# Performance work log

Measured on AMD Instinct MI355X. Metric: run time of the kernel, lower is better.

The kernel has to match this reference:

```python
import jax, jax.numpy as jnp
import numpy as np

B, T, D, H = 2, 2048, 2048, 16


def setup_inputs() -> dict:
    key = jax.random.key(0)
    ks = jax.random.split(key, 5)
    s = 0.02  # typical init scale
    return {
        "x": jax.random.normal(ks[0], (B, T, D), jnp.float32),
        "wq": jax.random.normal(ks[1], (D, D), jnp.float32) * s,
        "wk": jax.random.normal(ks[2], (D, D), jnp.float32) * s,
        "wv": jax.random.normal(ks[3], (D, D), jnp.float32) * s,
        "wo": jax.random.normal(ks[4], (D, D), jnp.float32) * s,
    }


def weight_quant(w):
    # BitNet ternary-ish quant: sign(w) * mean(|w|), straight-through estimator
    scale = jnp.maximum(jnp.mean(jnp.abs(w)), 1e-5)
    q = jnp.sign(w) * scale
    return jax.lax.stop_gradient(q) + w - jax.lax.stop_gradient(w)


def reference(x, wq, wk, wv, wo):
    b, t, c = x.shape
    h = H
    hd = c // h
    # F.linear: y = x @ w.T  (weight shape [out, in])
    def proj(w):
        y = jnp.einsum('btc,dc->btd', x, weight_quant(w))
        return y.reshape(b, t, h, hd).transpose(0, 2, 1, 3)  # [b,h,t,hd]

    q, k, v = proj(wq), proj(wk), proj(wv)
    scale = 1.0 / np.sqrt(hd).astype(np.float32)
    scores = jnp.einsum('bhqd,bhkd->bhqk', q, k) * scale
    causal = jnp.tril(jnp.ones((t, t), dtype=bool))
    scores = jnp.where(causal, scores, jnp.finfo(scores.dtype).min)
    att = jax.nn.softmax(scores, axis=-1)
    y = jnp.einsum('bhqk,bhkd->bhqd', att, v)
    y = y.transpose(0, 2, 1, 3).reshape(b, t, c)
    return jnp.einsum('btc,dc->btd', y, weight_quant(wo))
```

## Files before the change

### kernel.cpp

```cpp
#include <hip/hip_runtime.h>
#include <stdint.h>

#define D_MODEL 2048
#define SEQ     2048
#define BATCH   2
#define NH      16
#define HD      128
#define M_TOT   (BATCH*SEQ)
#define NELEM_W (D_MODEL*D_MODEL)

typedef float f32x4 __attribute__((ext_vector_type(4)));
typedef short bf16x8 __attribute__((ext_vector_type(8)));

__device__ __forceinline__ unsigned short f2bf(float f) {
  union { float f; uint32_t u; } v; v.f = f;
  uint32_t r = v.u + 0x7FFFu + ((v.u >> 16) & 1u);
  return (unsigned short)(r >> 16);
}

__device__ __forceinline__ void gload_lds16(const unsigned short* g, unsigned short* l) {
  __builtin_amdgcn_global_load_lds(
      (const __attribute__((address_space(1))) unsigned int*)g,
      (__attribute__((address_space(3))) unsigned int*)l, 16, 0, 0);
}

__global__ __launch_bounds__(256) void sign_w(const float* w0, const float* w1,
                                              const float* w2, const float* w3,
                                              unsigned short* signs, float* partials) {
  const int wi = blockIdx.y;
  const float* w = (wi == 0) ? w0 : (wi == 1) ? w1 : (wi == 2) ? w2 : w3;
  unsigned short* o = signs + (size_t)wi * NELEM_W;
  const int t = threadIdx.x;
  const int i = blockIdx.x * 256 + t;
  float4 v = ((const float4*)w)[i];
  ushort4 s;
  s.x = (v.x > 0.f) ? 0x3F80u : ((v.x < 0.f) ? 0xBF80u : 0u);
  s.y = (v.y > 0.f) ? 0x3F80u : ((v.y < 0.f) ? 0xBF80u : 0u);
  s.z = (v.z > 0.f) ? 0x3F80u : ((v.z < 0.f) ? 0xBF80u : 0u);
  s.w = (v.w > 0.f) ? 0x3F80u : ((v.w < 0.f) ? 0xBF80u : 0u);
  ((ushort4*)o)[i] = s;
  float a = fabsf(v.x) + fabsf(v.y) + fabsf(v.z) + fabsf(v.w);
  #pragma unroll
  for (int off = 32; off; off >>= 1) a += __shfl_down(a, off);
  __shared__ float sm[4];
  if ((t & 63) == 0) sm[t >> 6] = a;
  __syncthreads();
  if (t == 0) partials[wi * 4096 + blockIdx.x] = sm[0] + sm[1] + sm[2] + sm[3];
}

__global__ __launch_bounds__(256) void reduce2(const float* partials, float* scales) {
  const int wi = blockIdx.x, t = threadIdx.x;
  float s = 0.f;
  #pragma unroll
  for (int i = 0; i < 16; ++i) s += partials[wi * 4096 + i * 256 + t];
  #pragma unroll
  for (int off = 32; off; off >>= 1) s += __shfl_down(s, off);
  __shared__ float sm[4];
  if ((t & 63) == 0) sm[t >> 6] = s;
  __syncthreads();
  if (t == 0) scales[wi] = fmaxf((sm[0] + sm[1] + sm[2] + sm[3]) * (1.f / 4194304.f), 1e-5f);
}

__global__ __launch_bounds__(256) void cvt_x(const float* x, unsigned short* xb) {
  const int i = blockIdx.x * 256 + threadIdx.x;
  float4 v = ((const float4*)x)[i];
  ushort4 o;
  o.x = f2bf(v.x); o.y = f2bf(v.y); o.z = f2bf(v.z); o.w = f2bf(v.w);
  ((ushort4*)xb)[i] = o;
}

template <int MODE>
__global__ __launch_bounds__(512, 2) void gemm_p(const unsigned short* __restrict__ A,
                                                 const unsigned short* __restrict__ W,
                                                 unsigned short* __restrict__ Qb,
                                                 unsigned short* __restrict__ Kb,
                                                 unsigned short* __restrict__ Vt,
                                                 float* __restrict__ outf,
                                                 const float* __restrict__ scales) {
  constexpr int K = 2048;
  constexpr int NT = 32;
  constexpr int BUF = 24576;
  __shared__ alignas(16) unsigned short lds[3 * BUF];
  const int t = threadIdx.x;
  const int wid = t >> 6, lane = t & 63;
  const int llo = lane & 15, lhi = lane >> 4;
  const int wm = wid >> 2, wn = wid & 3;
  (void)wm; (void)wn;
  const int wmr = wid >> 1, wnr = wid & 1;

  const int nwg = gridDim.x;
  const int bid = blockIdx.x;
  const int sid = (bid & 7) * (nwg >> 3) + (bid >> 3);
  const int mt = sid & 15, nt_ = sid >> 4;
  const int m0 = mt * 256;
  const int n0w = nt_ * 128;

  auto stageA = [&](int buf, int kt) {
    const int k0 = kt * 64;
    #pragma unroll
    for (int i = 0; i < 4; ++i) {
      const int c = i * 512 + t;
      const int row = c >> 3, slot = c & 7;
      gload_lds16(A + (size_t)(m0 + row) * K + k0 + ((slot ^ (row & 7)) << 3),
                  &lds[buf * BUF + (i * 512 + wid * 64) * 8]);
    }
  };
  auto stageB = [&](int buf, int kt) {
    const int k0 = kt * 64;
    #pragma unroll
    for (int i = 0; i < 2; ++i) {
      const int c = i * 512 + t;
      const int row = c >> 3, slot = c & 7;
      gload_lds16(W + (size_t)(n0w + row) * K + k0 + ((slot ^ (row & 7)) << 3),
                  &lds[buf * BUF + 16384 + (i * 512 + wid * 64) * 8]);
    }
  };

  f32x4 acc[4][4] = {};

  stageA(0, 0); stageB(0, 0);
  stageA(1, 1); stageB(1, 1);
  asm volatile("s_waitcnt vmcnt(6)" ::: "memory");
  __builtin_amdgcn_s_barrier();

  for (int kt = 0; kt < NT; ++kt) {
    const int cur = kt % 3;
    const int nb3 = (kt + 2) % 3;
    const bool pf = (kt + 2) < NT;
    if (pf) { stageA(nb3, kt + 2); stageB(nb3, kt + 2); }
    bf16x8 a[4][2], b[4][2];
    #pragma unroll
    for (int f = 0; f < 4; ++f) {
      const int ra = wmr * 64 + f * 16 + llo;
      #pragma unroll
      for (int kk = 0; kk < 2; ++kk)
        a[f][kk] = *(const bf16x8*)&lds[cur * BUF + ra * 64 + (((kk * 4 + lhi) ^ (ra & 7)) << 3)];
    }
    #pragma unroll
    for (int f = 0; f < 4; ++f) {
      const int rb = wnr * 64 + f * 16 + llo;
      #pragma unroll
      for (int kk = 0; kk < 2; ++kk)
        b[f][kk] = *(const bf16x8*)&lds[cur * BUF + 16384 + rb * 64 + (((kk * 4 + lhi) ^ (rb & 7)) << 3)];
    }
    __builtin_amdgcn_s_setprio(1);
    #pragma unroll
    for (int kk = 0; kk < 2; ++kk)
      #pragma unroll
      for (int fm = 0; fm < 4; ++fm)
        #pragma unroll
        for (int fn = 0; fn < 4; ++fn)
          acc[fm][fn] = __builtin_amdgcn_mfma_f32_16x16x32_bf16(a[fm][kk], b[fn][kk], acc[fm][fn], 0, 0, 0);
    __builtin_amdgcn_s_setprio(0);
    if (kt < NT - 1) {
      if (kt <= NT - 3) asm volatile("s_waitcnt vmcnt(6)" ::: "memory");
      else              asm volatile("s_waitcnt vmcnt(0)" ::: "memory");
      __builtin_amdgcn_s_barrier();
    }
  }

  if (MODE == 1) {
    const float sc = scales[3];
    #pragma unroll
    for (int fm = 0; fm < 4; ++fm)
      #pragma unroll
      for (int fn = 0; fn < 4; ++fn)
        #pragma unroll
        for (int r = 0; r < 4; ++r) {
          const int row = m0 + wmr * 64 + fm * 16 + lhi * 4 + r;
          const int col = n0w + wnr * 64 + fn * 16 + llo;
          outf[(size_t)row * D_MODEL + col] = acc[fm][fn][r] * sc;
        }
  } else {
    const int region = n0w >> 11;
    const int c0 = (n0w & 2047) + wnr * 64;
    const float sc = scales[region] * (region == 0 ? 0.08838834764831845f : 1.f);
    unsigned short* outb = (region == 0) ? Qb : (region == 1) ? Kb : Vt;
    #pragma unroll
    for (int fm = 0; fm < 4; ++fm)
      #pragma unroll
      for (int fn = 0; fn < 4; ++fn)
        #pragma unroll
        for (int r = 0; r < 4; ++r) {
          const int row = m0 + wmr * 64 + fm * 16 + lhi * 4 + r;
          const int colr = c0 + fn * 16 + llo;
          const int b_ = row >> 11, tt = row & 2047, h = colr >> 7, d = colr & 127;
          size_t idx;
          if (region < 2) idx = ((size_t)((b_ * NH + h) * SEQ + tt)) * HD + d;
          else            idx = ((size_t)((b_ * NH + h) * HD + d)) * SEQ + tt;
          outb[idx] = f2bf(acc[fm][fn][r] * sc);
        }
  }
}

__global__ __launch_bounds__(512, 4) void attn_fwd(const unsigned short* __restrict__ Q,
                                                   const unsigned short* __restrict__ Kt,
                                                   const unsigned short* __restrict__ VT,
                                                   unsigned short* __restrict__ O) {
  __shared__ alignas(16) unsigned short lds[2][16384];
  __shared__ alignas(16) unsigned short plds[8][1024];
  const int t = threadIdx.x;
  const int wid = t >> 6, lane = t & 63;
  const int llo = lane & 15, lhi = lane >> 4;
  const int j0 = blockIdx.x;
  int bh, g;
  if (j0 < 256) { bh = j0 & 31; g = 15 - (j0 >> 5); }
  else          { bh = (j0 - 256) & 31; g = (j0 - 256) >> 5; }
  const int qbase = g * 128;
  const int nt = 2 * g + 2;
  const size_t bh_td = (size_t)bh * SEQ * HD;
  const size_t bh_dt = (size_t)bh * HD * SEQ;
  unsigned short* pw = &plds[wid][0];
  const int fvl = (llo & 7) ^ ((llo & 8) >> 1);
  const int pkey = llo & 14;

  auto stage = [&](int buf, int j) {
    const int t0 = j * 64;
    #pragma unroll
    for (int i = 0; i < 2; ++i) {
      const int c = i * 512 + t;
      const int row = c >> 4, slot = c & 15;
      gload_lds16(Kt + bh_td + (size_t)(t0 + row) * HD + ((slot ^ (row & 15)) << 3),
                  &lds[buf][(size_t)(i * 512 + wid * 64) * 8]);
    }
    #pragma unroll
    for (int i = 0; i < 2; ++i) {
      const int c = i * 512 + t;
      const int vrow = c >> 3, vslot = c & 7;
      const int fv = (vrow & 7) ^ ((vrow & 8) >> 1);
      gload_lds16(VT + bh_dt + (size_t)vrow * SEQ + t0 + ((vslot ^ fv) << 3),
                  &lds[buf][8192 + (size_t)(i * 512 + wid * 64) * 8]);
    }
  };

  bf16x8 qa[4];
  {
    const unsigned short* qp = Q + bh_td + (size_t)(qbase + wid * 16 + llo) * HD + lhi * 8;
    #pragma unroll
    for (int kk = 0; kk < 4; ++kk) qa[kk] = *(const bf16x8*)(qp + kk * 32);
  }
  f32x4 oacc[8] = {};
  float m_r = -1e30f, l_r = 0.f;

  stage(0, 0);
  for (int j = 0; j < nt; ++j) {
    const int cur = j & 1;
    __syncthreads();
    if (j + 1 < nt) stage(cur ^ 1, j + 1);
    f32x4 s[4] = {};
    __builtin_amdgcn_s_setprio(1);
    #pragma unroll
    for (int nb = 0; nb < 4; ++nb) {
      const int row = nb * 16 + llo;
      #pragma unroll
      for (int kk = 0; kk < 4; ++kk) {
        const bf16x8 kb = *(const bf16x8*)&lds[cur][row * 128 + (((kk * 4 + lhi) ^ llo) << 3)];
        s[nb] = __builtin_amdgcn_mfma_f32_16x16x32_bf16(kb, qa[kk], s[nb], 0, 0, 0);
      }
    }
    __builtin_amdgcn_s_setprio(0);
    if (j >= nt - 2) {
      const int q = qbase + wid * 16 + llo;
      #pragma unroll
      for (int nb = 0; nb < 4; ++nb)
        #pragma unroll
        for (int r = 0; r < 4; ++r)
          if (j * 64 + nb * 16 + lhi * 4 + r > q) s[nb][r] = -1e30f;
    }
    float mloc = -1e30f;
    #pragma unroll
    for (int nb = 0; nb < 4; ++nb)
      #pragma unroll
      for (int r = 0; r < 4; ++r) mloc = fmaxf(mloc, s[nb][r]);
    mloc = fmaxf(mloc, __shfl_xor(mloc, 16));
    mloc = fmaxf(mloc, __shfl_xor(mloc, 32));
    float alq = 1.f;
    if (__any(mloc > m_r + 8.f)) {
      const float mn = fmaxf(m_r, mloc);
      alq = __expf(m_r - mn);
      m_r = mn;
      float alr[4];
      #pragma unroll
      for (int r = 0; r < 4; ++r) alr[r] = __shfl(alq, lhi * 4 + r);
      #pragma unroll
      for (int db = 0; db < 8; ++db)
        #pragma unroll
        for (int r = 0; r < 4; ++r) oacc[db][r] *= alr[r];
    }
    float ps = 0.f;
    #pragma unroll
    for (int nb = 0; nb < 4; ++nb) {
      const float p0 = __expf(s[nb][0] - m_r), p1 = __expf(s[nb][1] - m_r);
      const float p2 = __expf(s[nb][2] - m_r), p3 = __expf(s[nb][3] - m_r);
      ps += (p0 + p1) + (p2 + p3);
      uint2 uu;
      uu.x = (uint32_t)f2bf(p0) | ((uint32_t)f2bf(p1) << 16);
      uu.y = (uint32_t)f2bf(p2) | ((uint32_t)f2bf(p3) << 16);
      *(uint2*)&pw[llo * 64 + (((nb * 4 + lhi) ^ pkey) << 2)] = uu;
    }
    ps += __shfl_xor(ps, 16);
    ps += __shfl_xor(ps, 32);
    l_r = l_r * alq + ps;
    asm volatile("s_waitcnt lgkmcnt(0)" ::: "memory");
    __builtin_amdgcn_sched_barrier(0);
    const bf16x8 pa0 = *(const bf16x8*)&pw[llo * 64 + (((lhi * 2) ^ pkey) << 2)];
    const bf16x8 pa1 = *(const bf16x8*)&pw[llo * 64 + (((8 + lhi * 2) ^ pkey) << 2)];
    __builtin_amdgcn_s_setprio(1);
    #pragma unroll
    for (int db = 0; db < 8; ++db) {
      const unsigned short* vbp = &lds[cur][8192 + (db * 16 + llo) * 64];
      const bf16x8 vb0 = *(const bf16x8*)&vbp[(lhi ^ fvl) << 3];
      const bf16x8 vb1 = *(const bf16x8*)&vbp[((4 + lhi) ^ fvl) << 3];
      oacc[db] = __builtin_amdgcn_mfma_f32_16x16x32_bf16(pa0, vb0, oacc[db], 0, 0, 0);
      oacc[db] = __builtin_amdgcn_mfma_f32_16x16x32_bf16(pa1, vb1, oacc[db], 0, 0, 0);
    }
    __builtin_amdgcn_s_setprio(0);
  }

  const int b = bh >> 4, h = bh & 15;
  const float invq = 1.f / l_r;
  float invr[4];
  #pragma unroll
  for (int r = 0; r < 4; ++r) invr[r] = __shfl(invq, lhi * 4 + r);
  #pragma unroll
  for (int db = 0; db < 8; ++db)
    #pragma unroll
    for (int r = 0; r < 4; ++r) {
      const int qi = qbase + wid * 16 + lhi * 4 + r;
      const int d = db * 16 + llo;
      O[((size_t)(b * SEQ + qi)) * D_MODEL + h * HD + d] = f2bf(oacc[db][r] * invr[r]);
    }
}

extern "C" void kernel_launch(void* const* d_in, const int* in_sizes, int n_in,
                              void* d_out, int out_size, void* d_ws, size_t ws_size,
                              hipStream_t stream) {
  const float* x  = (const float*)d_in[0];
  const float* wq = (const float*)d_in[1];
  const float* wk = (const float*)d_in[2];
  const float* wv = (const float*)d_in[3];
  const float* wo = (const float*)d_in[4];

  char* ws = (char*)d_ws;
  float* scales   = (float*)ws;
  float* partials = (float*)(ws + 256);
  unsigned short* xbf   = (unsigned short*)(ws + 131072);
  const size_t nMD = (size_t)M_TOT * D_MODEL;
  unsigned short* signs = xbf + nMD;
  unsigned short* Qb = signs + 4 * (size_t)NELEM_W;
  unsigned short* Kb = Qb + nMD;
  unsigned short* Vt = Kb + nMD;
  unsigned short* Ab = Vt + nMD;

  sign_w<<<dim3(4096, 4), 256, 0, stream>>>(wq, wk, wv, wo, signs, partials);
  reduce2<<<dim3(4), 256, 0, stream>>>(partials, scales);
  cvt_x<<<dim3(8192), 256, 0, stream>>>(x, xbf);

  gemm_p<0><<<dim3(768), 512, 0, stream>>>(xbf, signs, Qb, Kb, Vt, nullptr, scales);

  attn_fwd<<<dim3(512), 512, 0, stream>>>(Qb, Kb, Vt, Ab);

  gemm_p<1><<<dim3(256), 512, 0, stream>>>(Ab, signs + 3 * (size_t)NELEM_W,
                                           nullptr, nullptr, nullptr, (float*)d_out, scales);
}
```

Measured before the change: 263.7 us.

## Interleave LDS reads, global prefetch and MFMA in ping-pong phases in projection GEMM

Splits each k-tile iteration of the projection GEMM into four phases. Each phase loads a subset of A/B fragments from LDS, issues part of the next-tile global-to-LDS prefetch, then runs eight MFMAs, with workgroup barriers and sched_barriers between phases so loads and math alternate across the block. Launch bounds drop from 2 to 1 blocks per CU, which lets each block use more registers but halves residency. The added barriers add synchronization cost in exchange for explicit overlap of memory and matrix work.

```diff
diff --git a/kernel.cpp b/kernel.cpp
--- a/kernel.cpp
+++ b/kernel.cpp
@@ -70,7 +70,7 @@
 }
 
 template <int MODE>
-__global__ __launch_bounds__(512, 2) void gemm_p(const unsigned short* __restrict__ A,
+__global__ __launch_bounds__(512, 1) void gemm_p(const unsigned short* __restrict__ A,
                                                  const unsigned short* __restrict__ W,
                                                  unsigned short* __restrict__ Qb,
                                                  unsigned short* __restrict__ Kb,
@@ -84,8 +84,6 @@
   const int t = threadIdx.x;
   const int wid = t >> 6, lane = t & 63;
   const int llo = lane & 15, lhi = lane >> 4;
-  const int wm = wid >> 2, wn = wid & 3;
-  (void)wm; (void)wn;
   const int wmr = wid >> 1, wnr = wid & 1;
 
   const int nwg = gridDim.x;
@@ -95,10 +93,10 @@
   const int m0 = mt * 256;
   const int n0w = nt_ * 128;
 
-  auto stageA = [&](int buf, int kt) {
+  auto stageA_h = [&](int buf, int kt, int half) {
     const int k0 = kt * 64;
     #pragma unroll
-    for (int i = 0; i < 4; ++i) {
+    for (int i = half * 2; i < half * 2 + 2; ++i) {
       const int c = i * 512 + t;
       const int row = c >> 3, slot = c & 7;
       gload_lds16(A + (size_t)(m0 + row) * K + k0 + ((slot ^ (row & 7)) << 3),
@@ -118,8 +116,14 @@
 
   f32x4 acc[4][4] = {};
 
-  stageA(0, 0); stageB(0, 0);
-  stageA(1, 1); stageB(1, 1);
+  #define LDA_(cur, f, kk) (*(const bf16x8*)&lds[(cur) * BUF + (wmr * 64 + (f) * 16 + llo) * 64 + \
+      ((((kk) * 4 + lhi) ^ ((wmr * 64 + (f) * 16 + llo) & 7)) << 3)])
+  #define LDB_(cur, f, kk) (*(const bf16x8*)&lds[(cur) * BUF + 16384 + (wnr * 64 + (f) * 16 + llo) * 64 + \
+      ((((kk) * 4 + lhi) ^ ((wnr * 64 + (f) * 16 + llo) & 7)) << 3)])
+  #define MFMA_(d, x, y) d = __builtin_amdgcn_mfma_f32_16x16x32_bf16(x, y, d, 0, 0, 0)
+
+  stageA_h(0, 0, 0); stageA_h(0, 0, 1); stageB(0, 0);
+  stageA_h(1, 1, 0); stageA_h(1, 1, 1); stageB(1, 1);
   asm volatile("s_waitcnt vmcnt(6)" ::: "memory");
   __builtin_amdgcn_s_barrier();
 
@@ -127,30 +131,55 @@
     const int cur = kt % 3;
     const int nb3 = (kt + 2) % 3;
     const bool pf = (kt + 2) < NT;
-    if (pf) { stageA(nb3, kt + 2); stageB(nb3, kt + 2); }
-    bf16x8 a[4][2], b[4][2];
-    #pragma unroll
-    for (int f = 0; f < 4; ++f) {
-      const int ra = wmr * 64 + f * 16 + llo;
-      #pragma unroll
-      for (int kk = 0; kk < 2; ++kk)
-        a[f][kk] = *(const bf16x8*)&lds[cur * BUF + ra * 64 + (((kk * 4 + lhi) ^ (ra & 7)) << 3)];
-    }
-    #pragma unroll
-    for (int f = 0; f < 4; ++f) {
-      const int rb = wnr * 64 + f * 16 + llo;
-      #pragma unroll
-      for (int kk = 0; kk < 2; ++kk)
-        b[f][kk] = *(const bf16x8*)&lds[cur * BUF + 16384 + rb * 64 + (((kk * 4 + lhi) ^ (rb & 7)) << 3)];
-    }
-    __builtin_amdgcn_s_setprio(1);
-    #pragma unroll
-    for (int kk = 0; kk < 2; ++kk)
-      #pragma unroll
-      for (int fm = 0; fm < 4; ++fm)
-        #pragma unroll
-        for (int fn = 0; fn < 4; ++fn)
-          acc[fm][fn] = __builtin_amdgcn_mfma_f32_16x16x32_bf16(a[fm][kk], b[fn][kk], acc[fm][fn], 0, 0, 0);
+    bf16x8 va0 = LDA_(cur, 0, 0), va1 = LDA_(cur, 1, 0);
+    bf16x8 vb0 = LDB_(cur, 0, 0), vb1 = LDB_(cur, 1, 0);
+    bf16x8 vb2 = LDB_(cur, 2, 0), vb3 = LDB_(cur, 3, 0);
+    if (pf) stageA_h(nb3, kt + 2, 0);
+    __builtin_amdgcn_s_barrier();
+    asm volatile("s_waitcnt lgkmcnt(0)" ::: "memory");
+    __builtin_amdgcn_sched_barrier(0);
+    __builtin_amdgcn_s_setprio(1);
+    MFMA_(acc[0][0], va0, vb0); MFMA_(acc[0][1], va0, vb1);
+    MFMA_(acc[0][2], va0, vb2); MFMA_(acc[0][3], va0, vb3);
+    MFMA_(acc[1][0], va1, vb0); MFMA_(acc[1][1], va1, vb1);
+    MFMA_(acc[1][2], va1, vb2); MFMA_(acc[1][3], va1, vb3);
+    __builtin_amdgcn_s_setprio(0);
+    __builtin_amdgcn_s_barrier();
+    bf16x8 va2 = LDA_(cur, 2, 0), va3 = LDA_(cur, 3, 0);
+    if (pf) stageA_h(nb3, kt + 2, 1);
+    __builtin_amdgcn_s_barrier();
+    asm volatile("s_waitcnt lgkmcnt(0)" ::: "memory");
+    __builtin_amdgcn_sched_barrier(0);
+    __builtin_amdgcn_s_setprio(1);
+    MFMA_(acc[2][0], va2, vb0); MFMA_(acc[2][1], va2, vb1);
+    MFMA_(acc[2][2], va2, vb2); MFMA_(acc[2][3], va2, vb3);
+    MFMA_(acc[3][0], va3, vb0); MFMA_(acc[3][1], va3, vb1);
+    MFMA_(acc[3][2], va3, vb2); MFMA_(acc[3][3], va3, vb3);
+    __builtin_amdgcn_s_setprio(0);
+    __builtin_amdgcn_s_barrier();
+    va0 = LDA_(cur, 0, 1); va1 = LDA_(cur, 1, 1);
+    vb0 = LDB_(cur, 0, 1); vb1 = LDB_(cur, 1, 1);
+    vb2 = LDB_(cur, 2, 1); vb3 = LDB_(cur, 3, 1);
+    if (pf) stageB(nb3, kt + 2);
+    __builtin_amdgcn_s_barrier();
+    asm volatile("s_waitcnt lgkmcnt(0)" ::: "memory");
+    __builtin_amdgcn_sched_barrier(0);
+    __builtin_amdgcn_s_setprio(1);
+    MFMA_(acc[0][0], va0, vb0); MFMA_(acc[0][1], va0, vb1);
+    MFMA_(acc[0][2], va0, vb2); MFMA_(acc[0][3], va0, vb3);
+    MFMA_(acc[1][0], va1, vb0); MFMA_(acc[1][1], va1, vb1);
+    MFMA_(acc[1][2], va1, vb2); MFMA_(acc[1][3], va1, vb3);
+    __builtin_amdgcn_s_setprio(0);
+    __builtin_amdgcn_s_barrier();
+    va2 = LDA_(cur, 2, 1); va3 = LDA_(cur, 3, 1);
+    __builtin_amdgcn_s_barrier();
+    asm volatile("s_waitcnt lgkmcnt(0)" ::: "memory");
+    __builtin_amdgcn_sched_barrier(0);
+    __builtin_amdgcn_s_setprio(1);
+    MFMA_(acc[2][0], va2, vb0); MFMA_(acc[2][1], va2, vb1);
+    MFMA_(acc[2][2], va2, vb2); MFMA_(acc[2][3], va2, vb3);
+    MFMA_(acc[3][0], va3, vb0); MFMA_(acc[3][1], va3, vb1);
+    MFMA_(acc[3][2], va3, vb2); MFMA_(acc[3][3], va3, vb3);
     __builtin_amdgcn_s_setprio(0);
     if (kt < NT - 1) {
       if (kt <= NT - 3) asm volatile("s_waitcnt vmcnt(6)" ::: "memory");
@@ -158,6 +187,9 @@
       __builtin_amdgcn_s_barrier();
     }
   }
+  #undef LDA_
+  #undef LDB_
+  #undef MFMA_
 
   if (MODE == 1) {
     const float sc = scales[3];
```

Result: no change. 265.1 us (+0.5%).

## Use four-wave GEMM blocks with larger per-wave 128x64 output tiles

Applied to the files above, without the earlier changes.

The projection GEMM now runs with 256 threads (4 waves) per block instead of 512, and each wave computes a 128x64 tile with 32 accumulators instead of 64x64. Staging loops issue twice as many loads per thread, and the vmcnt waits are adjusted to match. LDS fragment loads are interleaved per k-step, and the s_setprio hints are dropped. The aim is more MFMA work per LDS fragment read and less per-wave overhead. The cost is fewer waves for latency hiding, higher register pressure under launch_bounds(256,1), and possibly lower occupancy.

```diff
diff --git a/kernel.cpp b/kernel.cpp
--- a/kernel.cpp
+++ b/kernel.cpp
@@ -70,7 +70,7 @@
 }
 
 template <int MODE>
-__global__ __launch_bounds__(512, 2) void gemm_p(const unsigned short* __restrict__ A,
+__global__ __launch_bounds__(256, 1) void gemm_p(const unsigned short* __restrict__ A,
                                                  const unsigned short* __restrict__ W,
                                                  unsigned short* __restrict__ Qb,
                                                  unsigned short* __restrict__ Kb,
@@ -84,9 +84,7 @@
   const int t = threadIdx.x;
   const int wid = t >> 6, lane = t & 63;
   const int llo = lane & 15, lhi = lane >> 4;
-  const int wm = wid >> 2, wn = wid & 3;
-  (void)wm; (void)wn;
-  const int wmr = wid >> 1, wnr = wid & 1;
+  const int wm = wid >> 1, wn = wid & 1;
 
   const int nwg = gridDim.x;
   const int bid = blockIdx.x;
@@ -98,29 +96,29 @@
   auto stageA = [&](int buf, int kt) {
     const int k0 = kt * 64;
     #pragma unroll
-    for (int i = 0; i < 4; ++i) {
-      const int c = i * 512 + t;
+    for (int i = 0; i < 8; ++i) {
+      const int c = i * 256 + t;
       const int row = c >> 3, slot = c & 7;
       gload_lds16(A + (size_t)(m0 + row) * K + k0 + ((slot ^ (row & 7)) << 3),
-                  &lds[buf * BUF + (i * 512 + wid * 64) * 8]);
+                  &lds[buf * BUF + (i * 256 + wid * 64) * 8]);
     }
   };
   auto stageB = [&](int buf, int kt) {
     const int k0 = kt * 64;
     #pragma unroll
-    for (int i = 0; i < 2; ++i) {
-      const int c = i * 512 + t;
+    for (int i = 0; i < 4; ++i) {
+      const int c = i * 256 + t;
       const int row = c >> 3, slot = c & 7;
       gload_lds16(W + (size_t)(n0w + row) * K + k0 + ((slot ^ (row & 7)) << 3),
-                  &lds[buf * BUF + 16384 + (i * 512 + wid * 64) * 8]);
+                  &lds[buf * BUF + 16384 + (i * 256 + wid * 64) * 8]);
     }
   };
 
-  f32x4 acc[4][4] = {};
+  f32x4 acc[8][4] = {};
 
   stageA(0, 0); stageB(0, 0);
   stageA(1, 1); stageB(1, 1);
-  asm volatile("s_waitcnt vmcnt(6)" ::: "memory");
+  asm volatile("s_waitcnt vmcnt(12)" ::: "memory");
   __builtin_amdgcn_s_barrier();
 
   for (int kt = 0; kt < NT; ++kt) {
@@ -128,33 +126,28 @@
     const int nb3 = (kt + 2) % 3;
     const bool pf = (kt + 2) < NT;
     if (pf) { stageA(nb3, kt + 2); stageB(nb3, kt + 2); }
-    bf16x8 a[4][2], b[4][2];
-    #pragma unroll
-    for (int f = 0; f < 4; ++f) {
-      const int ra = wmr * 64 + f * 16 + llo;
-      #pragma unroll
-      for (int kk = 0; kk < 2; ++kk)
-        a[f][kk] = *(const bf16x8*)&lds[cur * BUF + ra * 64 + (((kk * 4 + lhi) ^ (ra & 7)) << 3)];
-    }
-    #pragma unroll
-    for (int f = 0; f < 4; ++f) {
-      const int rb = wnr * 64 + f * 16 + llo;
-      #pragma unroll
-      for (int kk = 0; kk < 2; ++kk)
-        b[f][kk] = *(const bf16x8*)&lds[cur * BUF + 16384 + rb * 64 + (((kk * 4 + lhi) ^ (rb & 7)) << 3)];
-    }
-    __builtin_amdgcn_s_setprio(1);
-    #pragma unroll
-    for (int kk = 0; kk < 2; ++kk)
-      #pragma unroll
-      for (int fm = 0; fm < 4; ++fm)
+    #pragma unroll
+    for (int kk = 0; kk < 2; ++kk) {
+      bf16x8 a[8], b[4];
+      #pragma unroll
+      for (int f = 0; f < 8; ++f) {
+        const int ra = wm * 128 + f * 16 + llo;
+        a[f] = *(const bf16x8*)&lds[cur * BUF + ra * 64 + (((kk * 4 + lhi) ^ (ra & 7)) << 3)];
+      }
+      #pragma unroll
+      for (int f = 0; f < 4; ++f) {
+        const int rb = wn * 64 + f * 16 + llo;
+        b[f] = *(const bf16x8*)&lds[cur * BUF + 16384 + rb * 64 + (((kk * 4 + lhi) ^ (rb & 7)) << 3)];
+      }
+      #pragma unroll
+      for (int fm = 0; fm < 8; ++fm)
         #pragma unroll
         for (int fn = 0; fn < 4; ++fn)
-          acc[fm][fn] = __builtin_amdgcn_mfma_f32_16x16x32_bf16(a[fm][kk], b[fn][kk], acc[fm][fn], 0, 0, 0);
-    __builtin_amdgcn_s_setprio(0);
+          acc[fm][fn] = __builtin_amdgcn_mfma_f32_16x16x32_bf16(a[fm], b[fn], acc[fm][fn], 0, 0, 0);
+    }
     if (kt < NT - 1) {
-      if (kt <= NT - 3) asm volatile("s_waitcnt vmcnt(6)" ::: "memory");
-      else              asm volatile("s_waitcnt vmcnt(0)" ::: "memory");
+      if (pf) asm volatile("s_waitcnt vmcnt(12)" ::: "memory");
+      else    asm volatile("s_waitcnt vmcnt(0)" ::: "memory");
       __builtin_amdgcn_s_barrier();
     }
   }
@@ -162,27 +155,27 @@
   if (MODE == 1) {
     const float sc = scales[3];
     #pragma unroll
-    for (int fm = 0; fm < 4; ++fm)
+    for (int fm = 0; fm < 8; ++fm)
       #pragma unroll
       for (int fn = 0; fn < 4; ++fn)
         #pragma unroll
         for (int r = 0; r < 4; ++r) {
-          const int row = m0 + wmr * 64 + fm * 16 + lhi * 4 + r;
-          const int col = n0w + wnr * 64 + fn * 16 + llo;
+          const int row = m0 + wm * 128 + fm * 16 + lhi * 4 + r;
+          const int col = n0w + wn * 64 + fn * 16 + llo;
           outf[(size_t)row * D_MODEL + col] = acc[fm][fn][r] * sc;
         }
   } else {
     const int region = n0w >> 11;
-    const int c0 = (n0w & 2047) + wnr * 64;
+    const int c0 = (n0w & 2047) + wn * 64;
     const float sc = scales[region] * (region == 0 ? 0.08838834764831845f : 1.f);
     unsigned short* outb = (region == 0) ? Qb : (region == 1) ? Kb : Vt;
     #pragma unroll
-    for (int fm = 0; fm < 4; ++fm)
+    for (int fm = 0; fm < 8; ++fm)
       #pragma unroll
       for (int fn = 0; fn < 4; ++fn)
         #pragma unroll
         for (int r = 0; r < 4; ++r) {
-          const int row = m0 + wmr * 64 + fm * 16 + lhi * 4 + r;
+          const int row = m0 + wm * 128 + fm * 16 + lhi * 4 + r;
           const int colr = c0 + fn * 16 + llo;
           const int b_ = row >> 11, tt = row & 2047, h = colr >> 7, d = colr & 127;
           size_t idx;
@@ -356,10 +349,10 @@
   reduce2<<<dim3(4), 256, 0, stream>>>(partials, scales);
   cvt_x<<<dim3(8192), 256, 0, stream>>>(x, xbf);
 
-  gemm_p<0><<<dim3(768), 512, 0, stream>>>(xbf, signs, Qb, Kb, Vt, nullptr, scales);
+  gemm_p<0><<<dim3(768), 256, 0, stream>>>(xbf, signs, Qb, Kb, Vt, nullptr, scales);
 
   attn_fwd<<<dim3(512), 512, 0, stream>>>(Qb, Kb, Vt, Ab);
 
-  gemm_p<1><<<dim3(256), 512, 0, stream>>>(Ab, signs + 3 * (size_t)NELEM_W,
+  gemm_p<1><<<dim3(256), 256, 0, stream>>>(Ab, signs + 3 * (size_t)NELEM_W,
                                            nullptr, nullptr, nullptr, (float*)d_out, scales);
 }
```

Result: slower. 303.3 us (+15.0%).
